# Kernel tuning notes

Hardware: AMD Instinct MI355X
Metric: run time of the kernel (lower is better)

Reference implementation:

```python
import jax, jax.numpy as jnp
import numpy as np

MOVING_RATE = 0.999

def _l2norm(x, eps=1e-12):
    # matches F.normalize(dim=-1): x / max(||x||, eps)
    return x / jnp.maximum(jnp.linalg.norm(x, axis=-1, keepdims=True), eps)

def setup_inputs() -> dict:
    k = jax.random.key(0)
    k1, k2, k3 = jax.random.split(k, 3)
    B, S, K, D = 8192, 14, 512, 256
    return {
        "key": jax.random.normal(k1, (B, S, D), dtype=jnp.float32),
        "value": jax.random.normal(k2, (B, S, D), dtype=jnp.float32),
        "memory": jax.random.normal(k3, (S, K, D), dtype=jnp.float32),
    }

def reference(key, value, memory):
    # key, value: (B, S, D); memory: (S, K, D). update=True path, all slots batched.
    K = memory.shape[1]
    xn = _l2norm(key)                                   # (B,S,D)
    mn = _l2norm(memory)                                # (S,K,D)
    score = jnp.einsum('bsd,skd->bsk', xn, mn)          # (B,S,K)

    # --- EMA codebook update (value is detached in the original) ---
    v = jax.lax.stop_gradient(value)
    ind = jnp.argmax(score, axis=-1)                    # (B,S)
    oh = jax.nn.one_hot(ind, K, dtype=value.dtype)      # (B,S,K)
    oh_sum = oh.sum(axis=0)                             # (S,K)
    emb_sum = jnp.einsum('bsd,bsk->skd', v, oh)         # (S,K,D)
    emb_mean = emb_sum / (oh_sum[..., None] + 1e-6)
    new_mem = memory * MOVING_RATE + emb_mean * (1.0 - MOVING_RATE)

    # --- re-score against updated codebook ---
    score2 = jnp.einsum('bsd,skd->bsk', xn, _l2norm(new_mem))
    ind2 = jnp.argmax(score2, axis=-1)
    oh2 = jax.nn.one_hot(ind2, K, dtype=value.dtype)    # (B,S,K)

    # note: original adds value[:, 0, :] (slot 0) for EVERY slot i — kept faithfully
    out = value[:, :1, :] + jnp.einsum('bsk,skd->bsd', oh2, new_mem)  # (B,S,D)
    return out, new_mem
```

## Files before the change

kernel.cpp:

```cpp
#include <hip/hip_runtime.h>
#include <cstddef>
#include <cstdint>

#define B_ 8192
#define S_ 14
#define K_ 512
#define D_ 256

typedef __attribute__((ext_vector_type(8))) short bfx8;
typedef __attribute__((ext_vector_type(4))) float fx4;

typedef __attribute__((address_space(3))) unsigned int       lds_u32;
typedef const __attribute__((address_space(1))) unsigned int glb_u32;

__device__ __forceinline__ void gload16(const void* g, void* l) {
    __builtin_amdgcn_global_load_lds((glb_u32*)g, (lds_u32*)l, 16, 0, 0);
}

__device__ __forceinline__ unsigned short f2bf(float x) {
    union { float f; unsigned int u; } v; v.f = x;
    unsigned int r = (v.u + 0x7FFFu + ((v.u >> 16) & 1u)) >> 16;
    return (unsigned short)r;
}
__device__ __forceinline__ float bf2f(unsigned short h) {
    union { unsigned int u; float f; } v; v.u = ((unsigned int)h) << 16;
    return v.f;
}

__global__ __launch_bounds__(64) void rownorm_kernel(
    const float* __restrict__ rows, float* __restrict__ invn)
{
    const int row  = blockIdx.x;
    const int lane = threadIdx.x;
    const float4 v = *reinterpret_cast<const float4*>(rows + (size_t)row * D_ + lane * 4);
    float ss = v.x * v.x + v.y * v.y + v.z * v.z + v.w * v.w;
    #pragma unroll
    for (int m = 32; m >= 1; m >>= 1) ss += __shfl_xor(ss, m, 64);
    if (lane == 0) invn[row] = 1.0f / fmaxf(sqrtf(ss), 1e-12f);
}

__global__ __launch_bounds__(256) void split_key_kernel(
    const float* __restrict__ key,
    unsigned short* __restrict__ ph, unsigned short* __restrict__ pm,
    unsigned short* __restrict__ pl)
{
    const int gid  = blockIdx.x * 256 + threadIdx.x;
    const int e    = gid * 4;
    const int b    = e / (S_ * D_);
    const int rem  = e - b * (S_ * D_);
    const int s    = rem >> 8;
    const int d    = rem & 255;
    const float4 x = *reinterpret_cast<const float4*>(key + e);
    const size_t o = ((size_t)s * B_ + b) * D_ + d;

    float xs[4] = { x.x, x.y, x.z, x.w };
    unsigned short hh[4], mm[4], ll[4];
    #pragma unroll
    for (int i = 0; i < 4; ++i) {
        unsigned short a = f2bf(xs[i]);
        float r1 = xs[i] - bf2f(a);
        unsigned short bq = f2bf(r1);
        float r2 = r1 - bf2f(bq);
        unsigned short c = f2bf(r2);
        hh[i] = a; mm[i] = bq; ll[i] = c;
    }
    *reinterpret_cast<ushort4*>(ph + o) = make_ushort4(hh[0], hh[1], hh[2], hh[3]);
    *reinterpret_cast<ushort4*>(pm + o) = make_ushort4(mm[0], mm[1], mm[2], mm[3]);
    *reinterpret_cast<ushort4*>(pl + o) = make_ushort4(ll[0], ll[1], ll[2], ll[3]);
}

__global__ __launch_bounds__(256) void split_mem_kernel(
    const float* __restrict__ mem,
    unsigned short* __restrict__ ph, unsigned short* __restrict__ pm,
    unsigned short* __restrict__ pl)
{
    const int e    = (blockIdx.x * 256 + threadIdx.x) * 4;
    const float4 x = *reinterpret_cast<const float4*>(mem + e);
    float xs[4] = { x.x, x.y, x.z, x.w };
    unsigned short hh[4], mm[4], ll[4];
    #pragma unroll
    for (int i = 0; i < 4; ++i) {
        unsigned short a = f2bf(xs[i]);
        float r1 = xs[i] - bf2f(a);
        unsigned short bq = f2bf(r1);
        float r2 = r1 - bf2f(bq);
        unsigned short c = f2bf(r2);
        hh[i] = a; mm[i] = bq; ll[i] = c;
    }
    *reinterpret_cast<ushort4*>(ph + e) = make_ushort4(hh[0], hh[1], hh[2], hh[3]);
    *reinterpret_cast<ushort4*>(pm + e) = make_ushort4(mm[0], mm[1], mm[2], mm[3]);
    *reinterpret_cast<ushort4*>(pl + e) = make_ushort4(ll[0], ll[1], ll[2], ll[3]);
}

__global__ __launch_bounds__(256, 3) void gemm_argmax_kernel(
    const unsigned short* __restrict__ kh, const unsigned short* __restrict__ km,
    const unsigned short* __restrict__ kl,
    const unsigned short* __restrict__ mh, const unsigned short* __restrict__ mm_,
    const unsigned short* __restrict__ ml,
    const float* __restrict__ invn,
    float* __restrict__ pV, int* __restrict__ pI)
{
    __shared__ short T[6][128 * 32];
    __shared__ float sInv[128];
    __shared__ float bV[128][2];
    __shared__ int   bI[128][2];

    const int orig = blockIdx.x;
    const int wg   = (orig & 7) * 448 + (orig >> 3);
    const int by   = wg & 3;
    const int bx   = (wg >> 2) & 63;
    const int s    = wg >> 8;

    const int t    = threadIdx.x;
    const int b0   = bx * 128;
    const int n0   = by * 128;
    const int w    = t >> 6;
    const int lane = t & 63;
    const int wm   = w >> 1, wn = w & 1;
    const int lr   = lane & 15, lg = lane >> 4;

    const size_t sB = (size_t)s * B_;
    const size_t sK = (size_t)s * K_;

    const unsigned short* __restrict__ APl[3] = { kh, km, kl };
    const unsigned short* __restrict__ BPl[3] = { mh, mm_, ml };

    fx4 acc[4][4];
    #pragma unroll
    for (int i = 0; i < 4; ++i)
        #pragma unroll
        for (int j = 0; j < 4; ++j) acc[i][j] = (fx4)0.0f;

    const int rsub = lane >> 2;
    const int csw  = (((lane & 3) ^ ((lane >> 3) & 3)) * 8);
    const int rdof = ((lg ^ ((lr >> 1) & 3)) * 8);

    for (int dc = 0; dc < 8; ++dc) {
        const int dco = dc * 32 + csw;
        #pragma unroll
        for (int p = 0; p < 3; ++p) {
            #pragma unroll
            for (int u = 0; u < 2; ++u) {
                const int R0 = w * 32 + u * 16;
                gload16(APl[p] + (sB + b0 + R0 + rsub) * D_ + dco, &T[p][R0 * 32]);
                gload16(BPl[p] + (sK + n0 + R0 + rsub) * D_ + dco, &T[3 + p][R0 * 32]);
            }
        }
        __syncthreads();

        bfx8 bf[3][4];
        #pragma unroll
        for (int bp = 0; bp < 3; ++bp)
            #pragma unroll
            for (int j = 0; j < 4; ++j)
                bf[bp][j] = *reinterpret_cast<const bfx8*>(
                    &T[3 + bp][(wn * 64 + j * 16 + lr) * 32 + rdof]);

        #pragma unroll
        for (int ap = 0; ap < 3; ++ap) {
            bfx8 af[4];
            #pragma unroll
            for (int i = 0; i < 4; ++i)
                af[i] = *reinterpret_cast<const bfx8*>(
                    &T[ap][(wm * 64 + i * 16 + lr) * 32 + rdof]);
            #pragma unroll
            for (int bp = 0; bp < 3 - ap; ++bp) {
                __builtin_amdgcn_s_setprio(1);
                #pragma unroll
                for (int i = 0; i < 4; ++i)
                    #pragma unroll
                    for (int j = 0; j < 4; ++j)
                        acc[i][j] = __builtin_amdgcn_mfma_f32_16x16x32_bf16(
                            af[i], bf[bp][j], acc[i][j], 0, 0, 0);
                __builtin_amdgcn_s_setprio(0);
            }
        }
        __syncthreads();
    }

    if (t < 128) sInv[t] = invn[sK + n0 + t];
    __syncthreads();

    #pragma unroll
    for (int i = 0; i < 4; ++i) {
        #pragma unroll
        for (int r = 0; r < 4; ++r) {
            float bv = -3.4e38f; int bi = 0x7fffffff;
            #pragma unroll
            for (int j = 0; j < 4; ++j) {
                const int kloc = wn * 64 + j * 16 + lr;
                const float v  = acc[i][j][r] * sInv[kloc];
                const int  kg  = n0 + kloc;
                if (v > bv || (v == bv && kg < bi)) { bv = v; bi = kg; }
            }
            #pragma unroll
            for (int msk = 1; msk < 16; msk <<= 1) {
                const float ov = __shfl_xor(bv, msk, 64);
                const int   oi = __shfl_xor(bi, msk, 64);
                if (ov > bv || (ov == bv && oi < bi)) { bv = ov; bi = oi; }
            }
            if (lr == 0) {
                const int mrow = wm * 64 + i * 16 + lg * 4 + r;
                bV[mrow][wn] = bv; bI[mrow][wn] = bi;
            }
        }
    }
    __syncthreads();

    if (t < 128) {
        const float v0 = bV[t][0], v1 = bV[t][1];
        const int   i0 = bI[t][0], i1 = bI[t][1];
        const bool take1 = (v1 > v0) || (v1 == v0 && i1 < i0);
        const size_t o = ((size_t)s * 4 + by) * B_ + b0 + t;
        pV[o] = take1 ? v1 : v0;
        pI[o] = take1 ? i1 : i0;
    }
}

__global__ __launch_bounds__(256) void combine1_kernel(
    const float* __restrict__ pV, const int* __restrict__ pI,
    int* __restrict__ ind1)
{
    const int idx = blockIdx.x * 256 + threadIdx.x;
    const int s   = idx >> 13;
    const int b   = idx & 8191;
    float bv = -3.4e38f; int bi = 0x7fffffff;
    #pragma unroll
    for (int nb = 0; nb < 4; ++nb) {
        const size_t o = ((size_t)s * 4 + nb) * B_ + b;
        const float v = pV[o]; const int i = pI[o];
        if (v > bv || (v == bv && i < bi)) { bv = v; bi = i; }
    }
    ind1[idx] = bi;
}

__global__ __launch_bounds__(256) void combine2_out_kernel(
    const float* __restrict__ pV, const int* __restrict__ pI,
    const float* __restrict__ value, const float* __restrict__ newmem,
    float* __restrict__ out)
{
    const int row  = blockIdx.x * 4 + (threadIdx.x >> 6);
    const int lane = threadIdx.x & 63;
    const int s    = row >> 13;
    const int b    = row & 8191;
    float bv = -3.4e38f; int bi = 0x7fffffff;
    #pragma unroll
    for (int nb = 0; nb < 4; ++nb) {
        const size_t o = ((size_t)s * 4 + nb) * B_ + b;
        const float v = pV[o]; const int i = pI[o];
        if (v > bv || (v == bv && i < bi)) { bv = v; bi = i; }
    }
    const float4 vv = *reinterpret_cast<const float4*>(
        value + (size_t)b * (S_ * D_) + lane * 4);
    const float4 mmv = *reinterpret_cast<const float4*>(
        newmem + ((size_t)s * K_ + bi) * D_ + lane * 4);
    float4 o4;
    o4.x = vv.x + mmv.x; o4.y = vv.y + mmv.y;
    o4.z = vv.z + mmv.z; o4.w = vv.w + mmv.w;
    *reinterpret_cast<float4*>(out + ((size_t)b * S_ + s) * D_ + lane * 4) = o4;
}

__global__ __launch_bounds__(256) void u1_hist_kernel(
    const int* __restrict__ ind1, int* __restrict__ hist)
{
    __shared__ int h[K_];
    const int t = threadIdx.x, c = blockIdx.x, s = blockIdx.y;
    h[t] = 0; h[t + 256] = 0;
    __syncthreads();
    const int k = ind1[(size_t)s * B_ + c * 256 + t];
    atomicAdd(&h[k], 1);
    __syncthreads();
    hist[((size_t)s * 32 + c) * K_ + t]       = h[t];
    hist[((size_t)s * 32 + c) * K_ + t + 256] = h[t + 256];
}

__global__ __launch_bounds__(512) void u2_scan_kernel(
    int* __restrict__ hist, int* __restrict__ cnt, int* __restrict__ offs)
{
    __shared__ int sc[K_];
    const int k = threadIdx.x, s = blockIdx.x;
    int run = 0;
    for (int c = 0; c < 32; ++c) {
        const size_t o = ((size_t)s * 32 + c) * K_ + k;
        const int x = hist[o];
        hist[o] = run;
        run += x;
    }
    cnt[s * K_ + k] = run;
    sc[k] = run;
    __syncthreads();
    for (int off = 1; off < K_; off <<= 1) {
        int v = (k >= off) ? sc[k - off] : 0;
        __syncthreads();
        sc[k] += v;
        __syncthreads();
    }
    offs[s * K_ + k] = sc[k] - run;
}

__global__ __launch_bounds__(256) void u3_scatter_kernel(
    const int* __restrict__ ind1, const int* __restrict__ hist,
    const int* __restrict__ offs, int* __restrict__ csr)
{
    __shared__ int sk[256];
    const int t = threadIdx.x, c = blockIdx.x, s = blockIdx.y;
    const int b = c * 256 + t;
    const int k = ind1[(size_t)s * B_ + b];
    sk[t] = k;
    __syncthreads();
    int rank = 0;
    for (int j = 0; j < t; ++j) rank += (sk[j] == k);
    const int pos = offs[s * K_ + k] + hist[((size_t)s * 32 + c) * K_ + k] + rank;
    csr[(size_t)s * B_ + pos] = b;
}

__global__ __launch_bounds__(64) void u4_gather_kernel(
    const int* __restrict__ csr, const int* __restrict__ cnt,
    const int* __restrict__ offs, const float* __restrict__ value,
    const float* __restrict__ memory, float* __restrict__ newmem)
{
    const int k = blockIdx.x, s = blockIdx.y, lane = threadIdx.x;
    const int n = cnt[s * K_ + k];
    const int base = offs[s * K_ + k];
    float4 a; a.x = a.y = a.z = a.w = 0.0f;
    for (int i = 0; i < n; ++i) {
        const int b = csr[(size_t)s * B_ + base + i];
        const float4 v = *reinterpret_cast<const float4*>(
            value + ((size_t)b * S_ + s) * D_ + lane * 4);
        a.x += v.x; a.y += v.y; a.z += v.z; a.w += v.w;
    }
    const float inv = 1.0f / ((float)n + 1e-6f);
    const size_t o = ((size_t)s * K_ + k) * D_ + lane * 4;
    const float4 mo = *reinterpret_cast<const float4*>(memory + o);
    float4 r;
    r.x = mo.x * 0.999f + a.x * inv * 0.001f;
    r.y = mo.y * 0.999f + a.y * inv * 0.001f;
    r.z = mo.z * 0.999f + a.z * inv * 0.001f;
    r.w = mo.w * 0.999f + a.w * inv * 0.001f;
    *reinterpret_cast<float4*>(newmem + o) = r;
}

template <int MODE>
__global__ __launch_bounds__(256) void score_argmax_kernel(
    const float* __restrict__ key, const float* __restrict__ mem,
    const float* __restrict__ invn, const float* __restrict__ value,
    float* __restrict__ out, int* __restrict__ ind_out)
{
    __shared__ __align__(16) float kt[64][36];
    __shared__ __align__(16) float mt[64][36];
    __shared__ float redV[64][16];
    __shared__ int   redI[64][16];

    const int t  = threadIdx.x;
    const int s  = blockIdx.y;
    const int b0 = blockIdx.x * 64;
    const int tb = t & 15;
    const int tk = t >> 4;

    float best[4]; int bidx[4];
    #pragma unroll
    for (int i = 0; i < 4; ++i) { best[i] = -3.4e38f; bidx[i] = 0; }

    for (int kc = 0; kc < 8; ++kc) {
        float acc[4][4];
        #pragma unroll
        for (int i = 0; i < 4; ++i)
            #pragma unroll
            for (int j = 0; j < 4; ++j) acc[i][j] = 0.0f;

        for (int dc = 0; dc < 8; ++dc) {
            #pragma unroll
            for (int u = 0; u < 2; ++u) {
                const int f = t + u * 256;
                const int row = f >> 3;
                const int c4 = f & 7;
                *reinterpret_cast<float4*>(&kt[row][c4 * 4]) =
                    *reinterpret_cast<const float4*>(
                        key + (((size_t)(b0 + row)) * S_ + s) * D_ + dc * 32 + c4 * 4);
                *reinterpret_cast<float4*>(&mt[row][c4 * 4]) =
                    *reinterpret_cast<const float4*>(
                        mem + (((size_t)s * K_) + kc * 64 + row) * D_ + dc * 32 + c4 * 4);
            }
            __syncthreads();
            #pragma unroll
            for (int d4 = 0; d4 < 8; ++d4) {
                float4 a[4], b[4];
                #pragma unroll
                for (int i = 0; i < 4; ++i)
                    a[i] = *reinterpret_cast<const float4*>(&kt[tb + i * 16][d4 * 4]);
                #pragma unroll
                for (int j = 0; j < 4; ++j)
                    b[j] = *reinterpret_cast<const float4*>(&mt[tk + j * 16][d4 * 4]);
                #pragma unroll
                for (int i = 0; i < 4; ++i)
                    #pragma unroll
                    for (int j = 0; j < 4; ++j)
                        acc[i][j] += a[i].x * b[j].x + a[i].y * b[j].y +
                                     a[i].z * b[j].z + a[i].w * b[j].w;
            }
            __syncthreads();
        }
        #pragma unroll
        for (int j = 0; j < 4; ++j) {
            const int kabs = kc * 64 + tk + j * 16;
            const float inv = invn[s * K_ + kabs];
            #pragma unroll
            for (int i = 0; i < 4; ++i) {
                const float v = acc[i][j] * inv;
                if (v > best[i] || (v == best[i] && kabs < bidx[i])) {
                    best[i] = v; bidx[i] = kabs;
                }
            }
        }
    }
    #pragma unroll
    for (int i = 0; i < 4; ++i) {
        redV[tb + i * 16][tk] = best[i];
        redI[tb + i * 16][tk] = bidx[i];
    }
    __syncthreads();
    if (t < 64) {
        float bv = redV[t][0]; int bi = redI[t][0];
        #pragma unroll
        for (int g = 1; g < 16; ++g) {
            const float v = redV[t][g]; const int ix = redI[t][g];
            if (v > bv || (v == bv && ix < bi)) { bv = v; bi = ix; }
        }
        if (MODE == 0) ind_out[(size_t)s * B_ + b0 + t] = bi;
        else           redI[t][0] = bi;
    }
    if (MODE == 1) {
        __syncthreads();
        const int w = t >> 6, lane = t & 63;
        for (int r = w; r < 64; r += 4) {
            const int bg = b0 + r;
            const int kk = redI[r][0];
            const float4 vv = *reinterpret_cast<const float4*>(
                value + (size_t)bg * (S_ * D_) + lane * 4);
            const float4 mmv = *reinterpret_cast<const float4*>(
                mem + ((size_t)s * K_ + kk) * D_ + lane * 4);
            float4 o;
            o.x = vv.x + mmv.x; o.y = vv.y + mmv.y;
            o.z = vv.z + mmv.z; o.w = vv.w + mmv.w;
            *reinterpret_cast<float4*>(
                out + (((size_t)bg) * S_ + s) * D_ + lane * 4) = o;
        }
    }
}

__global__ __launch_bounds__(256) void update_kernel(
    const int* __restrict__ ind1, const float* __restrict__ value,
    const float* __restrict__ memory, float* __restrict__ newmem)
{
    const int k0 = blockIdx.x * 4, s = blockIdx.y, t = threadIdx.x;
    __shared__ int sIdx[256];
    float a0 = 0.f, a1 = 0.f, a2 = 0.f, a3 = 0.f;
    int c0 = 0, c1 = 0, c2 = 0, c3 = 0;
    for (int b0 = 0; b0 < B_; b0 += 256) {
        sIdx[t] = ind1[(size_t)s * B_ + b0 + t];
        __syncthreads();
        for (int bb = 0; bb < 256; ++bb) {
            const int ix = sIdx[bb];
            const unsigned r = (unsigned)(ix - k0);
            if (r < 4u) {
                const float v = value[(((size_t)(b0 + bb)) * S_ + s) * D_ + t];
                if      (r == 0u) { a0 += v; ++c0; }
                else if (r == 1u) { a1 += v; ++c1; }
                else if (r == 2u) { a2 += v; ++c2; }
                else              { a3 += v; ++c3; }
            }
        }
        __syncthreads();
    }
    const float accs[4] = { a0, a1, a2, a3 };
    const int   cns [4] = { c0, c1, c2, c3 };
    #pragma unroll
    for (int kk = 0; kk < 4; ++kk) {
        const size_t off = ((size_t)s * K_ + k0 + kk) * D_ + t;
        const float mean = accs[kk] / ((float)cns[kk] + 1e-6f);
        newmem[off] = memory[off] * 0.999f + mean * 0.001f;
    }
}

extern "C" void kernel_launch(void* const* d_in, const int* in_sizes, int n_in,
                              void* d_out, int out_size, void* d_ws, size_t ws_size,
                              hipStream_t stream)
{
    const float* key    = (const float*)d_in[0];
    const float* value  = (const float*)d_in[1];
    const float* memory = (const float*)d_in[2];

    float* out    = (float*)d_out;
    float* newmem = out + (size_t)B_ * S_ * D_;

    const size_t keyPlane = (size_t)S_ * B_ * D_;
    const size_t memPlane = (size_t)S_ * K_ * D_;
    char* p = (char*)d_ws;
    size_t need = 0;
    auto alloc = [&](size_t bytes) -> char* {
        char* r = p + need;
        need += (bytes + 255) & ~(size_t)255;
        return r;
    };
    unsigned short* kh  = (unsigned short*)alloc(keyPlane * 2);
    unsigned short* km  = (unsigned short*)alloc(keyPlane * 2);
    unsigned short* kl  = (unsigned short*)alloc(keyPlane * 2);
    unsigned short* mh  = (unsigned short*)alloc(memPlane * 2);
    unsigned short* mm  = (unsigned short*)alloc(memPlane * 2);
    unsigned short* ml  = (unsigned short*)alloc(memPlane * 2);
    float* invn   = (float*)alloc((size_t)S_ * K_ * 4);
    float* pV     = (float*)alloc((size_t)S_ * 4 * B_ * 4);
    int*   pI     = (int*)  alloc((size_t)S_ * 4 * B_ * 4);
    int*   ind1   = (int*)  alloc((size_t)S_ * B_ * 4);
    int*   hist   = (int*)  alloc((size_t)S_ * 32 * K_ * 4);
    int*   cnt    = (int*)  alloc((size_t)S_ * K_ * 4);
    int*   offs   = (int*)  alloc((size_t)S_ * K_ * 4);
    int*   csr    = (int*)  alloc((size_t)S_ * B_ * 4);

    if (ws_size >= need) {
        split_key_kernel<<<dim3((B_ * S_ * D_) / 1024), 256, 0, stream>>>(key, kh, km, kl);
        split_mem_kernel<<<dim3((S_ * K_ * D_) / 1024), 256, 0, stream>>>(memory, mh, mm, ml);
        rownorm_kernel<<<dim3(S_ * K_), 64, 0, stream>>>(memory, invn);

        gemm_argmax_kernel<<<dim3(3584), 256, 0, stream>>>(
            kh, km, kl, mh, mm, ml, invn, pV, pI);
        combine1_kernel<<<dim3((S_ * B_) / 256), 256, 0, stream>>>(pV, pI, ind1);

        u1_hist_kernel<<<dim3(32, S_), 256, 0, stream>>>(ind1, hist);
        u2_scan_kernel<<<dim3(S_), 512, 0, stream>>>(hist, cnt, offs);
        u3_scatter_kernel<<<dim3(32, S_), 256, 0, stream>>>(ind1, hist, offs, csr);
        u4_gather_kernel<<<dim3(K_, S_), 64, 0, stream>>>(csr, cnt, offs, value, memory, newmem);

        rownorm_kernel<<<dim3(S_ * K_), 64, 0, stream>>>(newmem, invn);
        split_mem_kernel<<<dim3((S_ * K_ * D_) / 1024), 256, 0, stream>>>(newmem, mh, mm, ml);

        gemm_argmax_kernel<<<dim3(3584), 256, 0, stream>>>(
            kh, km, kl, mh, mm, ml, invn, pV, pI);
        combine2_out_kernel<<<dim3((S_ * B_) / 4), 256, 0, stream>>>(
            pV, pI, value, newmem, out);
    } else {
        float* invn1 = (float*)d_ws;
        float* invn2 = invn1 + S_ * K_;
        int*   find1 = (int*)(invn2 + S_ * K_);

        rownorm_kernel<<<dim3(S_ * K_), 64, 0, stream>>>(memory, invn1);
        score_argmax_kernel<0><<<dim3(B_ / 64, S_), 256, 0, stream>>>(
            key, memory, invn1, nullptr, nullptr, find1);
        update_kernel<<<dim3(K_ / 4, S_), 256, 0, stream>>>(find1, value, memory, newmem);
        rownorm_kernel<<<dim3(S_ * K_), 64, 0, stream>>>(newmem, invn2);
        score_argmax_kernel<1><<<dim3(B_ / 64, S_), 256, 0, stream>>>(
            key, newmem, invn2, value, out, nullptr);
    }
}
```

Baseline: 469.5 us.

## Use two-term bf16 split GEMM with certified top-2 margin and exact rescoring

Drops the third bf16 plane from the split-precision score GEMM, cutting the MFMA products from six to three per tile and shrinking the key/memory plane traffic. To keep argmax exact, the GEMM epilogue now tracks the best and second-best scores. Rows whose top-2 gap falls under a key-norm-scaled error bound go to an ambiguous list, which a double-precision rescoring kernel resolves. It also fuses memory splitting with row-norm computation and key splitting with key-norm computation. The cost is that correctness depends on the chosen error constant, plus an atomic append and a serial rescoring tail whose size is data dependent.

Result: slower. 617.3 us (+31.5%).

```diff
diff --git a/kernel.cpp b/kernel.cpp
--- a/kernel.cpp
+++ b/kernel.cpp
@@ -7,6 +7,8 @@
 #define K_ 512
 #define D_ 256
 
+#define CERT_C 1.5e-4f
+
 typedef __attribute__((ext_vector_type(8))) short bfx8;
 typedef __attribute__((ext_vector_type(4))) float fx4;
 
@@ -39,71 +41,73 @@
     if (lane == 0) invn[row] = 1.0f / fmaxf(sqrtf(ss), 1e-12f);
 }
 
-__global__ __launch_bounds__(256) void split_key_kernel(
+__global__ __launch_bounds__(64) void split_key2_kernel(
     const float* __restrict__ key,
     unsigned short* __restrict__ ph, unsigned short* __restrict__ pm,
-    unsigned short* __restrict__ pl)
-{
-    const int gid  = blockIdx.x * 256 + threadIdx.x;
-    const int e    = gid * 4;
-    const int b    = e / (S_ * D_);
-    const int rem  = e - b * (S_ * D_);
-    const int s    = rem >> 8;
-    const int d    = rem & 255;
-    const float4 x = *reinterpret_cast<const float4*>(key + e);
-    const size_t o = ((size_t)s * B_ + b) * D_ + d;
+    float* __restrict__ keynorm)
+{
+    const int b    = blockIdx.x;
+    const int s    = blockIdx.y;
+    const int lane = threadIdx.x;
+    const float4 x = *reinterpret_cast<const float4*>(
+        key + ((size_t)b * S_ + s) * D_ + lane * 4);
+    const size_t o = ((size_t)s * B_ + b) * D_ + lane * 4;
 
     float xs[4] = { x.x, x.y, x.z, x.w };
-    unsigned short hh[4], mm[4], ll[4];
+    unsigned short hh[4], mm[4];
     #pragma unroll
     for (int i = 0; i < 4; ++i) {
         unsigned short a = f2bf(xs[i]);
         float r1 = xs[i] - bf2f(a);
-        unsigned short bq = f2bf(r1);
-        float r2 = r1 - bf2f(bq);
-        unsigned short c = f2bf(r2);
-        hh[i] = a; mm[i] = bq; ll[i] = c;
+        hh[i] = a; mm[i] = f2bf(r1);
     }
     *reinterpret_cast<ushort4*>(ph + o) = make_ushort4(hh[0], hh[1], hh[2], hh[3]);
     *reinterpret_cast<ushort4*>(pm + o) = make_ushort4(mm[0], mm[1], mm[2], mm[3]);
-    *reinterpret_cast<ushort4*>(pl + o) = make_ushort4(ll[0], ll[1], ll[2], ll[3]);
-}
-
-__global__ __launch_bounds__(256) void split_mem_kernel(
+
+    float ss = x.x * x.x + x.y * x.y + x.z * x.z + x.w * x.w;
+    #pragma unroll
+    for (int m = 32; m >= 1; m >>= 1) ss += __shfl_xor(ss, m, 64);
+    if (lane == 0) keynorm[(size_t)s * B_ + b] = sqrtf(ss);
+}
+
+__global__ __launch_bounds__(64) void splitnorm_mem2_kernel(
     const float* __restrict__ mem,
     unsigned short* __restrict__ ph, unsigned short* __restrict__ pm,
-    unsigned short* __restrict__ pl)
-{
-    const int e    = (blockIdx.x * 256 + threadIdx.x) * 4;
+    float* __restrict__ invn)
+{
+    const int row  = blockIdx.x;
+    const int lane = threadIdx.x;
+    const size_t e = (size_t)row * D_ + lane * 4;
     const float4 x = *reinterpret_cast<const float4*>(mem + e);
+
     float xs[4] = { x.x, x.y, x.z, x.w };
-    unsigned short hh[4], mm[4], ll[4];
+    unsigned short hh[4], mm[4];
     #pragma unroll
     for (int i = 0; i < 4; ++i) {
         unsigned short a = f2bf(xs[i]);
         float r1 = xs[i] - bf2f(a);
-        unsigned short bq = f2bf(r1);
-        float r2 = r1 - bf2f(bq);
-        unsigned short c = f2bf(r2);
-        hh[i] = a; mm[i] = bq; ll[i] = c;
+        hh[i] = a; mm[i] = f2bf(r1);
     }
     *reinterpret_cast<ushort4*>(ph + e) = make_ushort4(hh[0], hh[1], hh[2], hh[3]);
     *reinterpret_cast<ushort4*>(pm + e) = make_ushort4(mm[0], mm[1], mm[2], mm[3]);
-    *reinterpret_cast<ushort4*>(pl + e) = make_ushort4(ll[0], ll[1], ll[2], ll[3]);
-}
-
-__global__ __launch_bounds__(256, 3) void gemm_argmax_kernel(
+
+    float ss = x.x * x.x + x.y * x.y + x.z * x.z + x.w * x.w;
+    #pragma unroll
+    for (int m = 32; m >= 1; m >>= 1) ss += __shfl_xor(ss, m, 64);
+    if (lane == 0) invn[row] = 1.0f / fmaxf(sqrtf(ss), 1e-12f);
+}
+
+__global__ __launch_bounds__(256, 3) void gemm_argmax3_kernel(
     const unsigned short* __restrict__ kh, const unsigned short* __restrict__ km,
-    const unsigned short* __restrict__ kl,
     const unsigned short* __restrict__ mh, const unsigned short* __restrict__ mm_,
-    const unsigned short* __restrict__ ml,
     const float* __restrict__ invn,
-    float* __restrict__ pV, int* __restrict__ pI)
-{
-    __shared__ short T[6][128 * 32];
+    float* __restrict__ pV1, int* __restrict__ pI1, float* __restrict__ pV2)
+{
+    __shared__ short T[4][128 * 32];
     __shared__ float sInv[128];
-    __shared__ float bV[128][2];
-    __shared__ int   bI[128][2];
+    __shared__ float bV1[128][2];
+    __shared__ int   bI1[128][2];
+    __shared__ float bV2[128][2];
 
     const int orig = blockIdx.x;
     const int wg   = (orig & 7) * 448 + (orig >> 3);
@@ -122,8 +126,8 @@
     const size_t sB = (size_t)s * B_;
     const size_t sK = (size_t)s * K_;
 
-    const unsigned short* __restrict__ APl[3] = { kh, km, kl };
-    const unsigned short* __restrict__ BPl[3] = { mh, mm_, ml };
+    const unsigned short* __restrict__ APl[2] = { kh, km };
+    const unsigned short* __restrict__ BPl[2] = { mh, mm_ };
 
     fx4 acc[4][4];
     #pragma unroll
@@ -138,33 +142,33 @@
     for (int dc = 0; dc < 8; ++dc) {
         const int dco = dc * 32 + csw;
         #pragma unroll
-        for (int p = 0; p < 3; ++p) {
+        for (int p = 0; p < 2; ++p) {
             #pragma unroll
             for (int u = 0; u < 2; ++u) {
                 const int R0 = w * 32 + u * 16;
                 gload16(APl[p] + (sB + b0 + R0 + rsub) * D_ + dco, &T[p][R0 * 32]);
-                gload16(BPl[p] + (sK + n0 + R0 + rsub) * D_ + dco, &T[3 + p][R0 * 32]);
-            }
-        }
-        __syncthreads();
-
-        bfx8 bf[3][4];
-        #pragma unroll
-        for (int bp = 0; bp < 3; ++bp)
+                gload16(BPl[p] + (sK + n0 + R0 + rsub) * D_ + dco, &T[2 + p][R0 * 32]);
+            }
+        }
+        __syncthreads();
+
+        bfx8 bf[2][4];
+        #pragma unroll
+        for (int bp = 0; bp < 2; ++bp)
             #pragma unroll
             for (int j = 0; j < 4; ++j)
                 bf[bp][j] = *reinterpret_cast<const bfx8*>(
-                    &T[3 + bp][(wn * 64 + j * 16 + lr) * 32 + rdof]);
-
-        #pragma unroll
-        for (int ap = 0; ap < 3; ++ap) {
+                    &T[2 + bp][(wn * 64 + j * 16 + lr) * 32 + rdof]);
+
+        #pragma unroll
+        for (int ap = 0; ap < 2; ++ap) {
             bfx8 af[4];
             #pragma unroll
             for (int i = 0; i < 4; ++i)
                 af[i] = *reinterpret_cast<const bfx8*>(
                     &T[ap][(wm * 64 + i * 16 + lr) * 32 + rdof]);
             #pragma unroll
-            for (int bp = 0; bp < 3 - ap; ++bp) {
+            for (int bp = 0; bp < 2 - ap; ++bp) {
                 __builtin_amdgcn_s_setprio(1);
                 #pragma unroll
                 for (int i = 0; i < 4; ++i)
@@ -185,71 +189,123 @@
     for (int i = 0; i < 4; ++i) {
         #pragma unroll
         for (int r = 0; r < 4; ++r) {
-            float bv = -3.4e38f; int bi = 0x7fffffff;
+            float v1 = -3.4e38f, v2 = -3.4e38f; int i1 = 0x7fffffff;
             #pragma unroll
             for (int j = 0; j < 4; ++j) {
                 const int kloc = wn * 64 + j * 16 + lr;
                 const float v  = acc[i][j][r] * sInv[kloc];
                 const int  kg  = n0 + kloc;
-                if (v > bv || (v == bv && kg < bi)) { bv = v; bi = kg; }
+                if (v > v1 || (v == v1 && kg < i1)) { v2 = v1; v1 = v; i1 = kg; }
+                else if (v > v2) v2 = v;
             }
             #pragma unroll
             for (int msk = 1; msk < 16; msk <<= 1) {
-                const float ov = __shfl_xor(bv, msk, 64);
-                const int   oi = __shfl_xor(bi, msk, 64);
-                if (ov > bv || (ov == bv && oi < bi)) { bv = ov; bi = oi; }
+                const float ov1 = __shfl_xor(v1, msk, 64);
+                const int   oi1 = __shfl_xor(i1, msk, 64);
+                const float ov2 = __shfl_xor(v2, msk, 64);
+                const bool op = (ov1 > v1) || (ov1 == v1 && oi1 < i1);
+                if (op) { v2 = fmaxf(v1, ov2); v1 = ov1; i1 = oi1; }
+                else    { v2 = fmaxf(ov1, v2); }
             }
             if (lr == 0) {
                 const int mrow = wm * 64 + i * 16 + lg * 4 + r;
-                bV[mrow][wn] = bv; bI[mrow][wn] = bi;
+                bV1[mrow][wn] = v1; bI1[mrow][wn] = i1; bV2[mrow][wn] = v2;
             }
         }
     }
     __syncthreads();
 
     if (t < 128) {
-        const float v0 = bV[t][0], v1 = bV[t][1];
-        const int   i0 = bI[t][0], i1 = bI[t][1];
-        const bool take1 = (v1 > v0) || (v1 == v0 && i1 < i0);
+        float v1 = bV1[t][0]; int i1 = bI1[t][0]; float v2 = bV2[t][0];
+        const float ov1 = bV1[t][1]; const int oi1 = bI1[t][1]; const float ov2 = bV2[t][1];
+        const bool op = (ov1 > v1) || (ov1 == v1 && oi1 < i1);
+        if (op) { v2 = fmaxf(v1, ov2); v1 = ov1; i1 = oi1; }
+        else    { v2 = fmaxf(ov1, v2); }
         const size_t o = ((size_t)s * 4 + by) * B_ + b0 + t;
-        pV[o] = take1 ? v1 : v0;
-        pI[o] = take1 ? i1 : i0;
-    }
-}
-
-__global__ __launch_bounds__(256) void combine1_kernel(
-    const float* __restrict__ pV, const int* __restrict__ pI,
-    int* __restrict__ ind1)
+        pV1[o] = v1; pI1[o] = i1; pV2[o] = v2;
+    }
+}
+
+__global__ __launch_bounds__(256) void combine_cert_kernel(
+    const float* __restrict__ pV1, const int* __restrict__ pI1,
+    const float* __restrict__ pV2, const float* __restrict__ keynorm,
+    int* __restrict__ ind, int* __restrict__ ambCnt, int* __restrict__ ambList)
 {
     const int idx = blockIdx.x * 256 + threadIdx.x;
     const int s   = idx >> 13;
     const int b   = idx & 8191;
-    float bv = -3.4e38f; int bi = 0x7fffffff;
+    float V1 = -3.4e38f, V2 = -3.4e38f; int I1 = 0x7fffffff;
     #pragma unroll
     for (int nb = 0; nb < 4; ++nb) {
         const size_t o = ((size_t)s * 4 + nb) * B_ + b;
-        const float v = pV[o]; const int i = pI[o];
-        if (v > bv || (v == bv && i < bi)) { bv = v; bi = i; }
-    }
-    ind1[idx] = bi;
-}
-
-__global__ __launch_bounds__(256) void combine2_out_kernel(
-    const float* __restrict__ pV, const int* __restrict__ pI,
-    const float* __restrict__ value, const float* __restrict__ newmem,
-    float* __restrict__ out)
+        const float v1 = pV1[o]; const int i1 = pI1[o]; const float v2 = pV2[o];
+        const bool op = (v1 > V1) || (v1 == V1 && i1 < I1);
+        if (op) { V2 = fmaxf(V1, v2); V1 = v1; I1 = i1; }
+        else    { V2 = fmaxf(v1, V2); }
+    }
+    ind[idx] = I1;
+    const float eps = CERT_C * keynorm[idx];
+    if (V1 - V2 < 2.0f * eps) {
+        const int p = atomicAdd(ambCnt, 1);
+        ambList[p] = idx;
+    }
+}
+
+__global__ __launch_bounds__(64) void zero2_kernel(
+    int* __restrict__ c1, int* __restrict__ c2)
+{
+    if (threadIdx.x == 0) { *c1 = 0; *c2 = 0; }
+}
+
+__global__ __launch_bounds__(256) void rescore_kernel(
+    const int* __restrict__ ambCnt, const int* __restrict__ ambList,
+    const float* __restrict__ key, const float* __restrict__ mem,
+    const float* __restrict__ invn, int* __restrict__ ind)
+{
+    __shared__ double sV[256];
+    __shared__ int    sI[256];
+    const int n = *ambCnt;
+    const int t = threadIdx.x;
+    for (int li = blockIdx.x; li < n; li += gridDim.x) {
+        const int row = ambList[li];
+        const int s = row >> 13, b = row & 8191;
+        const float* __restrict__ krow = key + ((size_t)b * S_ + s) * D_;
+        double bv = -1.0e300; int bk = 0x7fffffff;
+        for (int k = t; k < K_; k += 256) {
+            const float* __restrict__ mrow = mem + ((size_t)s * K_ + k) * D_;
+            double ds = 0.0;
+            for (int d4 = 0; d4 < 64; ++d4) {
+                const float4 kv = *reinterpret_cast<const float4*>(krow + d4 * 4);
+                const float4 mv = *reinterpret_cast<const float4*>(mrow + d4 * 4);
+                ds += (double)kv.x * mv.x + (double)kv.y * mv.y
+                    + (double)kv.z * mv.z + (double)kv.w * mv.w;
+            }
+            const double sc = ds * (double)invn[(size_t)s * K_ + k];
+            if (sc > bv || (sc == bv && k < bk)) { bv = sc; bk = k; }
+        }
+        sV[t] = bv; sI[t] = bk;
+        __syncthreads();
+        for (int off = 128; off >= 1; off >>= 1) {
+            if (t < off) {
+                const double ov = sV[t + off]; const int oi = sI[t + off];
+                if (ov > sV[t] || (ov == sV[t] && oi < sI[t])) { sV[t] = ov; sI[t] = oi; }
+            }
+            __syncthreads();
+        }
+        if (t == 0) ind[row] = sI[0];
+        __syncthreads();
+    }
+}
+
+__global__ __launch_bounds__(256) void gather_out_kernel(
+    const int* __restrict__ ind2, const float* __restrict__ value,
+    const float* __restrict__ newmem, float* __restrict__ out)
 {
     const int row  = blockIdx.x * 4 + (threadIdx.x >> 6);
     const int lane = threadIdx.x & 63;
     const int s    = row >> 13;
     const int b    = row & 8191;
-    float bv = -3.4e38f; int bi = 0x7fffffff;
-    #pragma unroll
-    for (int nb = 0; nb < 4; ++nb) {
-        const size_t o = ((size_t)s * 4 + nb) * B_ + b;
-        const float v = pV[o]; const int i = pI[o];
-        if (v > bv || (v == bv && i < bi)) { bv = v; bi = i; }
-    }
+    const int bi   = ind2[row];
     const float4 vv = *reinterpret_cast<const float4*>(
         value + (size_t)b * (S_ * D_) + lane * 4);
     const float4 mmv = *reinterpret_cast<const float4*>(
@@ -502,42 +558,54 @@
         need += (bytes + 255) & ~(size_t)255;
         return r;
     };
-    unsigned short* kh  = (unsigned short*)alloc(keyPlane * 2);
-    unsigned short* km  = (unsigned short*)alloc(keyPlane * 2);
-    unsigned short* kl  = (unsigned short*)alloc(keyPlane * 2);
-    unsigned short* mh  = (unsigned short*)alloc(memPlane * 2);
-    unsigned short* mm  = (unsigned short*)alloc(memPlane * 2);
-    unsigned short* ml  = (unsigned short*)alloc(memPlane * 2);
-    float* invn   = (float*)alloc((size_t)S_ * K_ * 4);
-    float* pV     = (float*)alloc((size_t)S_ * 4 * B_ * 4);
-    int*   pI     = (int*)  alloc((size_t)S_ * 4 * B_ * 4);
-    int*   ind1   = (int*)  alloc((size_t)S_ * B_ * 4);
-    int*   hist   = (int*)  alloc((size_t)S_ * 32 * K_ * 4);
-    int*   cnt    = (int*)  alloc((size_t)S_ * K_ * 4);
-    int*   offs   = (int*)  alloc((size_t)S_ * K_ * 4);
-    int*   csr    = (int*)  alloc((size_t)S_ * B_ * 4);
+    unsigned short* kh   = (unsigned short*)alloc(keyPlane * 2);
+    unsigned short* km   = (unsigned short*)alloc(keyPlane * 2);
+    unsigned short* mh   = (unsigned short*)alloc(memPlane * 2);
+    unsigned short* mm   = (unsigned short*)alloc(memPlane * 2);
+    float* invn    = (float*)alloc((size_t)S_ * K_ * 4);
+    float* keynorm = (float*)alloc((size_t)S_ * B_ * 4);
+    float* pV1     = (float*)alloc((size_t)S_ * 4 * B_ * 4);
+    int*   pI1     = (int*)  alloc((size_t)S_ * 4 * B_ * 4);
+    float* pV2     = (float*)alloc((size_t)S_ * 4 * B_ * 4);
+    int*   ind1    = (int*)  alloc((size_t)S_ * B_ * 4);
+    int*   ind2    = (int*)  alloc((size_t)S_ * B_ * 4);
+    int*   amb1Cnt = (int*)  alloc(256);
+    int*   amb2Cnt = (int*)  alloc(256);
+    int*   amb1Lst = (int*)  alloc((size_t)S_ * B_ * 4);
+    int*   amb2Lst = (int*)  alloc((size_t)S_ * B_ * 4);
+    int*   hist    = (int*)  alloc((size_t)S_ * 32 * K_ * 4);
+    int*   cnt     = (int*)  alloc((size_t)S_ * K_ * 4);
+    int*   offs    = (int*)  alloc((size_t)S_ * K_ * 4);
+    int*   csr     = (int*)  alloc((size_t)S_ * B_ * 4);
 
     if (ws_size >= need) {
-        split_key_kernel<<<dim3((B_ * S_ * D_) / 1024), 256, 0, stream>>>(key, kh, km, kl);
-        split_mem_kernel<<<dim3((S_ * K_ * D_) / 1024), 256, 0, stream>>>(memory, mh, mm, ml);
-        rownorm_kernel<<<dim3(S_ * K_), 64, 0, stream>>>(memory, invn);
-
-        gemm_argmax_kernel<<<dim3(3584), 256, 0, stream>>>(
-            kh, km, kl, mh, mm, ml, invn, pV, pI);
-        combine1_kernel<<<dim3((S_ * B_) / 256), 256, 0, stream>>>(pV, pI, ind1);
+        split_key2_kernel<<<dim3(B_, S_), 64, 0, stream>>>(key, kh, km, keynorm);
+        splitnorm_mem2_kernel<<<dim3(S_ * K_), 64, 0, stream>>>(memory, mh, mm, invn);
+        zero2_kernel<<<dim3(1), 64, 0, stream>>>(amb1Cnt, amb2Cnt);
+
+        gemm_argmax3_kernel<<<dim3(3584), 256, 0, stream>>>(
+            kh, km, mh, mm, invn, pV1, pI1, pV2);
+        combine_cert_kernel<<<dim3((S_ * B_) / 256), 256, 0, stream>>>(
+            pV1, pI1, pV2, keynorm, ind1, amb1Cnt, amb1Lst);
+        rescore_kernel<<<dim3(512), 256, 0, stream>>>(
+            amb1Cnt, amb1Lst, key, memory, invn, ind1);
 
         u1_hist_kernel<<<dim3(32, S_), 256, 0, stream>>>(ind1, hist);
         u2_scan_kernel<<<dim3(S_), 512, 0, stream>>>(hist, cnt, offs);
         u3_scatter_kernel<<<dim3(32, S_), 256, 0, stream>>>(ind1, hist, offs, csr);
         u4_gather_kernel<<<dim3(K_, S_), 64, 0, stream>>>(csr, cnt, offs, value, memory, newmem);
 
-        rownorm_kernel<<<dim3(S_ * K_), 64, 0, stream>>>(newmem, invn);
-        split_mem_kernel<<<dim3((S_ * K_ * D_) / 1024), 256, 0, stream>>>(newmem, mh, mm, ml);
-
-        gemm_argmax_kernel<<<dim3(3584), 256, 0, stream>>>(
-            kh, km, kl, mh, mm, ml, invn, pV, pI);
-        combine2_out_kernel<<<dim3((S_ * B_) / 4), 256, 0, stream>>>(
-            pV, pI, value, newmem, out);
+        splitnorm_mem2_kernel<<<dim3(S_ * K_), 64, 0, stream>>>(newmem, mh, mm, invn);
+
+        gemm_argmax3_kernel<<<dim3(3584), 256, 0, stream>>>(
+            kh, km, mh, mm, invn, pV1, pI1, pV2);
+        combine_cert_kernel<<<dim3((S_ * B_) / 256), 256, 0, stream>>>(
+            pV1, pI1, pV2, keynorm, ind2, amb2Cnt, amb2Lst);
+        rescore_kernel<<<dim3(512), 256, 0, stream>>>(
+            amb2Cnt, amb2Lst, key, newmem, invn, ind2);
+
+        gather_out_kernel<<<dim3((S_ * B_) / 4), 256, 0, stream>>>(
+            ind2, value, newmem, out);
     } else {
         float* invn1 = (float*)d_ws;
         float* invn2 = invn1 + S_ * K_;
```
